# Performance work log

Hardware: AMD Instinct MI355X
Metric: run time of the kernel (lower is better)

## Reference

```python
import jax, jax.numpy as jnp
import numpy as np

N = 100000      # nodes (patches)
NNZ = 800000    # incidence (node, hyperedge) pairs from H.coo()
E = 16384       # hyperedges
IN = 128        # in_dim == hidden_dim (residual path active)
HID = 128
HEADS = 4
HD = HID // HEADS   # 32, per-head out_dim
QD = 64             # type_query_dim
L = 2               # n_layers
NT = 4              # n_node_types
ET = 3              # n_edge_types


def setup_inputs() -> dict:
    key = jax.random.key(0)
    ks = jax.random.split(key, 12)
    f32 = jnp.float32
    return {
        "x": jax.random.normal(ks[0], (N, IN), f32),
        "node_types": jax.random.randint(ks[1], (N,), 0, NT, jnp.int32),
        "node_idx": jax.random.randint(ks[2], (NNZ,), 0, N, jnp.int32),
        "edge_idx": jax.random.randint(ks[3], (NNZ,), 0, E, jnp.int32),
        "edge_type": jax.random.randint(ks[4], (E,), 0, ET, jnp.int32),
        # per-layer, per-head parameters (leading axes L, HEADS)
        "type_query": (jax.random.normal(ks[5], (L, HEADS, NT, QD), f32) * 0.02),
        "fc1_w": jax.random.normal(ks[6], (L, HEADS, IN + QD, 32), f32) / np.sqrt(IN + QD),
        "fc1_b": jnp.zeros((L, HEADS, 32), f32),
        "fc2_w": jax.random.normal(ks[7], (L, HEADS, 32, 1), f32) / np.sqrt(32.0),
        "fc2_b": jnp.zeros((L, HEADS, 1), f32),
        "Wq": jax.random.normal(ks[8], (L, HEADS, IN, HD), f32) / np.sqrt(IN),
        "Wv": jax.random.normal(ks[9], (L, HEADS, IN, HD), f32) / np.sqrt(IN),
        "edge_ctx": jax.random.normal(ks[10], (L, HEADS, ET, HD), f32) * 0.02,
        "ln_g": jnp.ones((L, HID), f32),
        "ln_b": jnp.zeros((L, HID), f32),
    }


def _seg_softmax(a, seg, num):
    # scatter_softmax over segments `seg` (stable: subtract per-segment max)
    m = jax.ops.segment_max(a, seg, num_segments=num)
    ex = jnp.exp(a - m[seg])
    s = jax.ops.segment_sum(ex, seg, num_segments=num)
    return ex / s[seg]


def _head(h, node_types, node_idx, edge_idx, edge_type, tq, w1, b1, w2, b2, wq, wv, ec):
    # CascadedHyperGAT.forward, one head
    sig = tq[node_types]                                      # (N, QD)
    z = jnp.tanh(jnp.concatenate([h, sig], axis=1) @ w1 + b1)  # (N, 32)
    alpha_type = jax.nn.sigmoid(z @ w2 + b2)[:, 0]             # (N,)
    Q = h @ wq                                                 # (N, HD)
    V = h @ wv                                                 # (N, HD)
    ctx = ec[edge_type][edge_idx]                              # (NNZ, HD)
    a = jnp.sum(Q[node_idx] * ctx, axis=1)                     # (NNZ,)
    a = jnp.where(a >= 0, a, 0.2 * a)                          # leaky_relu(0.2)
    a = a * alpha_type[node_idx]
    attn = _seg_softmax(a, edge_idx, E)                        # (NNZ,)
    edge_feat = jax.ops.segment_sum(attn[:, None] * V[node_idx], edge_idx, num_segments=E)
    node_feat = jax.ops.segment_sum(attn[:, None] * edge_feat[edge_idx], node_idx, num_segments=N)
    return node_feat, edge_feat


def _layernorm(h, g, b, eps=1e-5):
    mu = h.mean(-1, keepdims=True)
    var = ((h - mu) ** 2).mean(-1, keepdims=True)
    return (h - mu) * jax.lax.rsqrt(var + eps) * g + b


def reference(x, node_types, node_idx, edge_idx, edge_type,
              type_query, fc1_w, fc1_b, fc2_w, fc2_b, Wq, Wv, edge_ctx, ln_g, ln_b):
    head_v = jax.vmap(_head, in_axes=(None, None, None, None, None, 0, 0, 0, 0, 0, 0, 0, 0))
    stats = [x]
    h = x
    for l in range(L):  # small static layer count
        nf, _ = head_v(h, node_types, node_idx, edge_idx, edge_type,
                       type_query[l], fc1_w[l], fc1_b[l], fc2_w[l], fc2_b[l],
                       Wq[l], Wv[l], edge_ctx[l])            # (HEADS, N, HD)
        hn = jnp.transpose(nf, (1, 0, 2)).reshape(h.shape[0], -1)  # concat heads -> (N, HID)
        if hn.shape == h.shape:
            hn = hn + h                                       # residual (dims match)
        h = _layernorm(hn, ln_g[l], ln_b[l])
        stats.append(h)
    return jnp.concatenate(stats, axis=-1)                    # (N, IN + HID*L)
```

## Files before the change

### kernel.cpp

```cpp
#include <hip/hip_runtime.h>
#include <math.h>

#define HEADS 4
#define HD 32
#define QD 64
#define DIN 128
#define NTYPES 4
#define ETYPES 3
#define CAP 512
#define WTC 272

typedef __attribute__((ext_vector_type(8))) short bf16x8;
typedef __attribute__((ext_vector_type(4))) float f32x4;
typedef unsigned short ushort_t;

static inline int cdiv(int a, int b){ return (a + b - 1) / b; }

__device__ inline unsigned short f2bf(float f){
  unsigned u = __float_as_uint(f);
  unsigned r = (u + 0x7FFF + ((u >> 16) & 1)) >> 16;
  return (unsigned short)r;
}
__device__ inline float bf2f(unsigned short u){ return __uint_as_float(((unsigned)u) << 16); }

__device__ inline float lgt_get(const ushort_t* __restrict__ lgt, int n, int et, int hh){
  uint2 lg = *(const uint2*)((const char*)lgt + (size_t)n*24 + et*8);
  unsigned u = (hh & 2) ? lg.y : lg.x;
  return bf2f((hh & 1) ? (ushort_t)(u >> 16) : (ushort_t)(u & 0xffff));
}


__global__ __launch_bounds__(256) void hist_k(const int* __restrict__ node_idx,
                                              const int* __restrict__ edge_idx,
                                              int* __restrict__ cnt,
                                              uint2* __restrict__ ranks, int E, int NNZ)
{
  int i = blockIdx.x*256 + threadIdx.x;
  if (i < NNZ){
    unsigned re = (unsigned)atomicAdd(&cnt[edge_idx[i]], 1);
    unsigned rn = (unsigned)atomicAdd(&cnt[E + node_idx[i]], 1);
    uint2 r; r.x = re; r.y = rn;
    ranks[i] = r;
  }
}

__global__ __launch_bounds__(1024) void scan_pass1(const int* __restrict__ in, int* __restrict__ bsums, int n)
{
  __shared__ int sd[1024];
  int i = blockIdx.x*1024 + threadIdx.x;
  sd[threadIdx.x] = (i < n) ? in[i] : 0;
  __syncthreads();
  for (int s = 512; s > 0; s >>= 1){
    if (threadIdx.x < s) sd[threadIdx.x] += sd[threadIdx.x + s];
    __syncthreads();
  }
  if (threadIdx.x == 0) bsums[blockIdx.x] = sd[0];
}

__global__ __launch_bounds__(1024) void scan_pass2(int* __restrict__ bsums, int nb)
{
  __shared__ int sd[1024];
  int v = (threadIdx.x < nb) ? bsums[threadIdx.x] : 0;
  sd[threadIdx.x] = v;
  __syncthreads();
  for (int s = 1; s < 1024; s <<= 1){
    int t = (threadIdx.x >= s) ? sd[threadIdx.x - s] : 0;
    __syncthreads();
    sd[threadIdx.x] += t;
    __syncthreads();
  }
  if (threadIdx.x < nb) bsums[threadIdx.x] = sd[threadIdx.x] - v;
}

__global__ __launch_bounds__(1024) void scan_pass3(const int* __restrict__ in, const int* __restrict__ bsums,
                                                   int* __restrict__ out, int n)
{
  __shared__ int sd[1024];
  int i = blockIdx.x*1024 + threadIdx.x;
  int v = (i < n) ? in[i] : 0;
  sd[threadIdx.x] = v;
  __syncthreads();
  for (int s = 1; s < 1024; s <<= 1){
    int t = (threadIdx.x >= s) ? sd[threadIdx.x - s] : 0;
    __syncthreads();
    sd[threadIdx.x] += t;
    __syncthreads();
  }
  if (i < n) out[i] = bsums[blockIdx.x] + sd[threadIdx.x] - v;
}

__global__ __launch_bounds__(256) void scatter_k(const int* __restrict__ node_idx, const int* __restrict__ edge_idx,
                                                 const uint2* __restrict__ ranks,
                                                 const int* __restrict__ off,
                                                 uint2* __restrict__ srtE_rec, int E, int NNZ)
{
  int i = blockIdx.x*256 + threadIdx.x;
  if (i >= NNZ) return;
  int n = node_idx[i], e = edge_idx[i];
  uint2 r = ranks[i];
  int pe = off[e] + (int)r.x;
  int pn = off[E + n] - NNZ + (int)r.y;
  uint2 rec; rec.x = (unsigned)n; rec.y = (unsigned)pn;
  srtE_rec[pe] = rec;
}


__global__ __launch_bounds__(128) void wtprep_k(const float* __restrict__ w1, const float* __restrict__ wv,
                                                short* __restrict__ Wt, int L)
{
  int c = blockIdx.x % 256, l = blockIdx.x / 256;
  int k = threadIdx.x;
  int hh = (c >> 5) & 3, j = c & 31;
  float v;
  if (c < 128) v = w1[((((size_t)l*HEADS + hh)*(DIN+QD)) + k)*32 + j];
  else         v = wv[((((size_t)l*HEADS + hh)*DIN) + k)*32 + j];
  Wt[((size_t)l*WTC + c)*128 + k] = (short)f2bf(v);
}

__global__ __launch_bounds__(128) void wqc_k(const float* __restrict__ wq, const float* __restrict__ ec,
                                             short* __restrict__ Wt)
{
  int b = blockIdx.x;
  int l = b / 12, c = b % 12, h = c / 3, et = c % 3;
  int k = threadIdx.x;
  const float* wrow = wq + ((((size_t)l*HEADS + h)*DIN) + k)*32;
  const float* ecp  = ec + (((size_t)l*HEADS + h)*ETYPES + et)*32;
  float s = 0.f;
  #pragma unroll
  for (int d = 0; d < 32; d++) s += wrow[d] * ecp[d];
  Wt[((size_t)l*WTC + 256 + c)*128 + k] = (short)f2bf(s);
}

__global__ __launch_bounds__(32) void sbias_k(const float* __restrict__ tq, const float* __restrict__ w1,
                                              const float* __restrict__ b1, float* __restrict__ sbias)
{
  int b = blockIdx.x;
  int ty = b % NTYPES; int hh = (b / NTYPES) % HEADS; int l = b / (NTYPES*HEADS);
  int j = threadIdx.x;
  const float* tqp = tq + (((size_t)l*HEADS + hh)*NTYPES + ty)*QD;
  const float* w1p = w1 + ((size_t)l*HEADS + hh)*(DIN+QD)*32;
  float s = b1[((size_t)l*HEADS + hh)*32 + j];
  for (int k = 0; k < QD; k++) s += tqp[k] * w1p[(size_t)(DIN + k)*32 + j];
  sbias[(size_t)b*32 + j] = s;
}


__device__ inline void load_afrag(const float* __restrict__ h, int hstride, int N,
                                  int rbase, int mf, int l15, int l4, int kk, bf16x8& a)
{
  int row = rbase + mf*16 + l15;
  int rr = (row < N) ? row : (N-1);
  const float* pa = h + (size_t)rr*hstride + kk*32 + l4*8;
  float4 f0 = *(const float4*)pa;
  float4 f1 = *(const float4*)(pa + 4);
  a[0] = (short)f2bf(f0.x); a[1] = (short)f2bf(f0.y);
  a[2] = (short)f2bf(f0.z); a[3] = (short)f2bf(f0.w);
  a[4] = (short)f2bf(f1.x); a[5] = (short)f2bf(f1.y);
  a[6] = (short)f2bf(f1.z); a[7] = (short)f2bf(f1.w);
}


__global__ __launch_bounds__(256) void gemm_f2(
    const float* __restrict__ h, int hstride,
    const short* __restrict__ Wt,
    const int* __restrict__ node_types,
    const float* __restrict__ sbias,
    const float* __restrict__ w2,
    const float* __restrict__ b2,
    ushort_t* __restrict__ lgt,
    ushort_t* __restrict__ vb,
    int N)
{
  __shared__ float alds[64][HEADS];
  int lane = threadIdx.x & 63, wvid = threadIdx.x >> 6;
  int l15 = lane & 15, l4 = lane >> 4;
  int rbase = blockIdx.x*64;
  int wtcol0 = (wvid < 2) ? wvid*64 : (128 + (wvid - 2)*64);

  f32x4 acc[4][4] = {};
  f32x4 acc_e[4] = {};

  #pragma unroll
  for (int kk = 0; kk < 4; kk++){
    bf16x8 a[4], b[4];
    #pragma unroll
    for (int mf = 0; mf < 4; mf++) load_afrag(h, hstride, N, rbase, mf, l15, l4, kk, a[mf]);
    #pragma unroll
    for (int cf = 0; cf < 4; cf++){
      int col = wtcol0 + cf*16 + l15;
      b[cf] = *(const bf16x8*)(Wt + (size_t)col*128 + kk*32 + l4*8);
    }
    #pragma unroll
    for (int mf = 0; mf < 4; mf++)
      #pragma unroll
      for (int cf = 0; cf < 4; cf++)
        acc[mf][cf] = __builtin_amdgcn_mfma_f32_16x16x32_bf16(a[mf], b[cf], acc[mf][cf], 0, 0, 0);
    if (wvid == 0){
      int ecol = 256 + ((l15 < 12) ? l15 : 11);
      bf16x8 be = *(const bf16x8*)(Wt + (size_t)ecol*128 + kk*32 + l4*8);
      #pragma unroll
      for (int mf = 0; mf < 4; mf++)
        acc_e[mf] = __builtin_amdgcn_mfma_f32_16x16x32_bf16(a[mf], be, acc_e[mf], 0, 0, 0);
    }
  }

  if (wvid < 2){
    #pragma unroll
    for (int mf = 0; mf < 4; mf++){
      int rw[4], ty[4];
      #pragma unroll
      for (int r = 0; r < 4; r++){
        rw[r] = rbase + mf*16 + l4*4 + r;
        ty[r] = (rw[r] < N) ? node_types[rw[r]] : 0;
      }
      #pragma unroll
      for (int p = 0; p < 2; p++){
        int hh = wvid*2 + p;
        float w2a = w2[hh*32 + l15];
        float w2b = w2[hh*32 + 16 + l15];
        float b2v = b2[hh];
        #pragma unroll
        for (int r = 0; r < 4; r++){
          const float* sb = sbias + ((size_t)hh*NTYPES + ty[r])*32;
          float z0 = acc[mf][2*p  ][r] + sb[l15];
          float z1 = acc[mf][2*p+1][r] + sb[16 + l15];
          float t0 = 1.f - 2.f/(__expf(2.f*z0) + 1.f);
          float t1 = 1.f - 2.f/(__expf(2.f*z1) + 1.f);
          float val = t0*w2a + t1*w2b;
          val += __shfl_xor(val, 1); val += __shfl_xor(val, 2);
          val += __shfl_xor(val, 4); val += __shfl_xor(val, 8);
          if (l15 == 0)
            alds[mf*16 + l4*4 + r][hh] = 1.f/(1.f + __expf(-(val + b2v)));
        }
      }
    }
  } else {
    #pragma unroll
    for (int mf = 0; mf < 4; mf++){
      #pragma unroll
      for (int r = 0; r < 4; r++){
        int row = rbase + mf*16 + l4*4 + r;
        if (row < N){
          #pragma unroll
          for (int cf = 0; cf < 4; cf++){
            int c = (wvid - 2)*64 + cf*16 + l15;
            int hh = c >> 5, d = c & 31;
            vb[((size_t)hh*N + row)*32 + d] = f2bf(acc[mf][cf][r]);
          }
        }
      }
    }
  }
  __syncthreads();

  if (wvid == 0 && l15 < 12){
    int hq = l15 / 3, et = l15 % 3;
    #pragma unroll
    for (int mf = 0; mf < 4; mf++){
      #pragma unroll
      for (int r = 0; r < 4; r++){
        int rowloc = mf*16 + l4*4 + r;
        int row = rbase + rowloc;
        if (row < N){
          float s = acc_e[mf][r] * alds[rowloc][hq];
          s = (s >= 0.f) ? s : 0.2f*s;
          lgt[(size_t)row*12 + et*4 + hq] = f2bf(s);
        }
      }
    }
  }
}


__global__ __launch_bounds__(256) void k2b_f(
    const ushort_t* __restrict__ lgt, const ushort_t* __restrict__ vb,
    const uint2* __restrict__ srtE_rec, const int* __restrict__ edge_off, const int* __restrict__ cnt_e,
    const int* __restrict__ edge_type,
    ushort_t* __restrict__ efb,
    uint4* __restrict__ attn_rec,
    int N, int E)
{
  __shared__ float lbuf[HEADS][CAP];
  __shared__ int   nbuf[CAP];
  __shared__ int   pnbuf[CAP];
  __shared__ float mi[HEADS][2];

  int e = blockIdx.x;
  int off = edge_off[e], cnt = cnt_e[e];
  if (cnt == 0) return;
  int lane = threadIdx.x & 63, hh = threadIdx.x >> 6;
  int g = lane & 15, grp = lane >> 4;
  int et = edge_type[e];

  if (cnt <= CAP){
    for (int j = threadIdx.x; j < cnt; j += 256){
      uint2 rc = srtE_rec[off + j];
      uint2 lg = *(const uint2*)((const char*)lgt + (size_t)rc.x*24 + et*8);
      lbuf[0][j] = bf2f((ushort_t)(lg.x & 0xffff));
      lbuf[1][j] = bf2f((ushort_t)(lg.x >> 16));
      lbuf[2][j] = bf2f((ushort_t)(lg.y & 0xffff));
      lbuf[3][j] = bf2f((ushort_t)(lg.y >> 16));
      nbuf[j] = (int)rc.x;
      pnbuf[j] = (int)rc.y;
    }
    __syncthreads();

    float mloc = -INFINITY;
    for (int j = lane; j < cnt; j += 64) mloc = fmaxf(mloc, lbuf[hh][j]);
    #pragma unroll
    for (int sh = 32; sh > 0; sh >>= 1) mloc = fmaxf(mloc, __shfl_xor(mloc, sh));
    float m = mloc;

    float ef0 = 0.f, ef1 = 0.f, ssum = 0.f;
    const int cm1 = cnt - 1;
    const ushort_t* vbh = vb + (size_t)hh*N*32;
    for (int jj = 0; jj < cnt; jj += 16){
      int j0 = jj + grp, j1 = j0 + 4, j2 = j0 + 8, j3 = j0 + 12;
      int n0 = nbuf[(j0 < cm1) ? j0 : cm1];
      int n1 = nbuf[(j1 < cm1) ? j1 : cm1];
      int n2 = nbuf[(j2 < cm1) ? j2 : cm1];
      int n3 = nbuf[(j3 < cm1) ? j3 : cm1];
      unsigned w0 = *(const unsigned*)&vbh[(size_t)n0*32 + 2*g];
      unsigned w1 = *(const unsigned*)&vbh[(size_t)n1*32 + 2*g];
      unsigned w2 = *(const unsigned*)&vbh[(size_t)n2*32 + 2*g];
      unsigned w3 = *(const unsigned*)&vbh[(size_t)n3*32 + 2*g];
      float e0 = (j0 < cnt) ? __expf(lbuf[hh][j0] - m) : 0.f;
      float e1 = (j1 < cnt) ? __expf(lbuf[hh][j1] - m) : 0.f;
      float e2 = (j2 < cnt) ? __expf(lbuf[hh][j2] - m) : 0.f;
      float e3 = (j3 < cnt) ? __expf(lbuf[hh][j3] - m) : 0.f;
      ef0 += e0*bf2f((ushort_t)(w0 & 0xffff)) + e1*bf2f((ushort_t)(w1 & 0xffff))
           + e2*bf2f((ushort_t)(w2 & 0xffff)) + e3*bf2f((ushort_t)(w3 & 0xffff));
      ef1 += e0*bf2f((ushort_t)(w0 >> 16)) + e1*bf2f((ushort_t)(w1 >> 16))
           + e2*bf2f((ushort_t)(w2 >> 16)) + e3*bf2f((ushort_t)(w3 >> 16));
      ssum += e0 + e1 + e2 + e3;
    }
    ef0 += __shfl_xor(ef0, 16); ef0 += __shfl_xor(ef0, 32);
    ef1 += __shfl_xor(ef1, 16); ef1 += __shfl_xor(ef1, 32);
    ssum += __shfl_xor(ssum, 16); ssum += __shfl_xor(ssum, 32);
    float inv = 1.0f / ssum;
    if (grp == 0){
      unsigned w = (unsigned)f2bf(ef0*inv) | ((unsigned)f2bf(ef1*inv) << 16);
      *(unsigned*)&efb[(size_t)e*128 + hh*32 + 2*g] = w;
    }
    if (lane == 0){ mi[hh][0] = m; mi[hh][1] = inv; }
    __syncthreads();

    if (hh == 0){
      for (int j = lane; j < cnt; j += 64){
        int pn = pnbuf[j];
        float a0 = __expf(lbuf[0][j] - mi[0][0]) * mi[0][1];
        float a1 = __expf(lbuf[1][j] - mi[1][0]) * mi[1][1];
        float a2 = __expf(lbuf[2][j] - mi[2][0]) * mi[2][1];
        float a3 = __expf(lbuf[3][j] - mi[3][0]) * mi[3][1];
        uint4 o;
        o.x = (unsigned)e;
        o.y = (unsigned)f2bf(a0) | ((unsigned)f2bf(a1) << 16);
        o.z = (unsigned)f2bf(a2) | ((unsigned)f2bf(a3) << 16);
        o.w = 0u;
        attn_rec[pn] = o;
      }
    }
  } else {
    float mloc = -INFINITY;
    for (int j = lane; j < cnt; j += 64)
      mloc = fmaxf(mloc, lgt_get(lgt, (int)srtE_rec[off + j].x, et, hh));
    #pragma unroll
    for (int sh = 32; sh > 0; sh >>= 1) mloc = fmaxf(mloc, __shfl_xor(mloc, sh));
    float m = mloc;

    float ef0 = 0.f, ef1 = 0.f, ssum = 0.f;
    for (int jj = 0; jj < cnt; jj += 4){
      int j = jj + grp;
      if (j < cnt){
        int n = (int)srtE_rec[off + j].x;
        float ex = __expf(lgt_get(lgt, n, et, hh) - m);
        unsigned vw = *(const unsigned*)&vb[((size_t)hh*N + n)*32 + 2*g];
        ef0 += ex * bf2f((unsigned short)(vw & 0xffff));
        ef1 += ex * bf2f((unsigned short)(vw >> 16));
        ssum += ex;
      }
    }
    ef0 += __shfl_xor(ef0, 16); ef0 += __shfl_xor(ef0, 32);
    ef1 += __shfl_xor(ef1, 16); ef1 += __shfl_xor(ef1, 32);
    ssum += __shfl_xor(ssum, 16); ssum += __shfl_xor(ssum, 32);
    float inv = 1.0f / ssum;
    if (grp == 0){
      unsigned w = (unsigned)f2bf(ef0*inv) | ((unsigned)f2bf(ef1*inv) << 16);
      *(unsigned*)&efb[(size_t)e*128 + hh*32 + 2*g] = w;
    }
    for (int j = lane; j < cnt; j += 64){
      uint2 rc = srtE_rec[off + j];
      float ex = __expf(lgt_get(lgt, (int)rc.x, et, hh) - m);
      ushort_t* p = (ushort_t*)&attn_rec[rc.y];
      p[2 + hh] = f2bf(ex * inv);
      if (hh == 0){
        ((unsigned*)p)[0] = (unsigned)e;
        ((unsigned*)p)[3] = 0u;
      }
    }
  }
}


__global__ __launch_bounds__(256) void k2c(
    const uint4* __restrict__ attn_rec,
    const int* __restrict__ node_off, const int* __restrict__ cnt_n, int noff_shift,
    const ushort_t* __restrict__ efb,
    const float* __restrict__ h_in, int hstride,
    const float* __restrict__ ln_g, const float* __restrict__ ln_b,
    float* __restrict__ out, int out_stride, int out_col, int do_xcopy, int N, int E)
{
  int wv = threadIdx.x >> 6, lane = threadIdx.x & 63;
  int n = blockIdx.x*4 + wv;
  if (n >= N) return;
  int off = node_off[n] - noff_shift, cnt = cnt_n[n];
  int hh = lane >> 4;
  float nf0 = 0.f, nf1 = 0.f;

  for (int j0 = 0; j0 < cnt; j0 += 8){
    int mm = cnt - j0; if (mm > 8) mm = 8;
    uint4 rc = make_uint4(0u, 0u, 0u, 0u);
    if (lane < mm) rc = attn_rec[off + j0 + lane];
    unsigned w[8]; float av[8];
    #pragma unroll
    for (int j = 0; j < 8; j++){
      unsigned ej = (unsigned)__shfl((int)rc.x, j);
      unsigned ay = (unsigned)__shfl((int)rc.y, j);
      unsigned az = (unsigned)__shfl((int)rc.z, j);
      unsigned u = (hh & 2) ? az : ay;
      float a = bf2f((hh & 1) ? (ushort_t)(u >> 16) : (ushort_t)(u & 0xffff));
      av[j] = (j < mm) ? a : 0.f;
      w[j] = *(const unsigned*)&efb[(size_t)ej*128 + 2*lane];
    }
    #pragma unroll
    for (int j = 0; j < 8; j++){
      nf0 += av[j] * bf2f((ushort_t)(w[j] & 0xffff));
      nf1 += av[j] * bf2f((ushort_t)(w[j] >> 16));
    }
  }

  float2 hr = *(const float2*)&h_in[(size_t)n*hstride + 2*lane];
  if (do_xcopy)
    *(float2*)&out[(size_t)n*out_stride + 2*lane] = hr;
  float hn0 = nf0 + hr.x, hn1 = nf1 + hr.y;

  float s = hn0 + hn1;
  #pragma unroll
  for (int sh = 32; sh > 0; sh >>= 1) s += __shfl_xor(s, sh);
  float mu = s * (1.0f/128.0f);
  float d0 = hn0 - mu, d1 = hn1 - mu;
  float s2 = d0*d0 + d1*d1;
  #pragma unroll
  for (int sh = 32; sh > 0; sh >>= 1) s2 += __shfl_xor(s2, sh);
  float r = rsqrtf(s2*(1.0f/128.0f) + 1e-5f);

  float2 g2 = *(const float2*)&ln_g[2*lane];
  float2 b2 = *(const float2*)&ln_b[2*lane];
  float2 o2;
  o2.x = d0*r*g2.x + b2.x;
  o2.y = d1*r*g2.y + b2.y;
  *(float2*)&out[(size_t)n*out_stride + out_col + 2*lane] = o2;
}


extern "C" void kernel_launch(void* const* d_in, const int* in_sizes, int n_in,
                              void* d_out, int out_size, void* d_ws, size_t ws_size,
                              hipStream_t stream)
{
  const float* x          = (const float*)d_in[0];
  const int*   node_types = (const int*)  d_in[1];
  const int*   node_idx   = (const int*)  d_in[2];
  const int*   edge_idx   = (const int*)  d_in[3];
  const int*   edge_type  = (const int*)  d_in[4];
  const float* type_query = (const float*)d_in[5];
  const float* fc1_w      = (const float*)d_in[6];
  const float* fc1_b      = (const float*)d_in[7];
  const float* fc2_w      = (const float*)d_in[8];
  const float* fc2_b      = (const float*)d_in[9];
  const float* Wq         = (const float*)d_in[10];
  const float* Wv         = (const float*)d_in[11];
  const float* edge_ctx   = (const float*)d_in[12];
  const float* ln_g       = (const float*)d_in[13];
  const float* ln_b       = (const float*)d_in[14];

  const int N   = in_sizes[1];
  const int NNZ = in_sizes[2];
  const int E   = in_sizes[4];
  const int L   = 2;
  const int EN  = E + N;

  char* ws = (char*)d_ws;
  size_t o = 0;
  auto alloc = [&](size_t bytes)->void*{
    void* p = ws + o;
    o = (o + bytes + 255) & ~(size_t)255;
    return p;
  };
  int* cnt       = (int*)alloc((size_t)EN*4);
  int* off       = (int*)alloc((size_t)(EN+1)*4);
  uint2* ranks   = (uint2*)alloc((size_t)NNZ*8);
  uint2* srtE_rec= (uint2*)alloc((size_t)NNZ*8);
  int* bsum      = (int*)alloc((size_t)1024*4);
  uint4* attn_rec = (uint4*)alloc((size_t)NNZ*16);
  ushort_t* vb      = (ushort_t*)alloc((size_t)HEADS*N*32*2);
  ushort_t* lgt     = (ushort_t*)alloc((size_t)N*12*2);
  ushort_t* efb     = (ushort_t*)alloc((size_t)E*128*2);
  short*    Wt      = (short*)alloc((size_t)L*WTC*128*2);
  float*    sbias   = (float*)alloc((size_t)L*HEADS*NTYPES*32*4);
  if (o > ws_size) return;

  hipMemsetAsync(cnt, 0, (size_t)EN*4, stream);

  hist_k<<<cdiv(NNZ,256),256,0,stream>>>(node_idx, edge_idx, cnt, ranks, E, NNZ);

  int nb = cdiv(EN,1024);
  scan_pass1<<<nb,1024,0,stream>>>(cnt, bsum, EN);
  scan_pass2<<<1,1024,0,stream>>>(bsum, nb);
  scan_pass3<<<nb,1024,0,stream>>>(cnt, bsum, off, EN);

  scatter_k<<<cdiv(NNZ,256),256,0,stream>>>(node_idx, edge_idx, ranks, off, srtE_rec, E, NNZ);

  wtprep_k<<<L*256,128,0,stream>>>(fc1_w, Wv, Wt, L);
  wqc_k<<<L*12,128,0,stream>>>(Wq, edge_ctx, Wt);
  sbias_k<<<L*HEADS*NTYPES,32,0,stream>>>(type_query, fc1_w, fc1_b, sbias);

  for (int l = 0; l < L; l++){
    const float* hin = (l == 0) ? x : ((const float*)d_out + 128);
    int hstride = (l == 0) ? DIN : (3*DIN);

    gemm_f2<<<cdiv(N,64),256,0,stream>>>(
        hin, hstride,
        Wt + (size_t)l*WTC*128,
        node_types,
        sbias + (size_t)l*HEADS*NTYPES*32,
        fc2_w + (size_t)l*HEADS*32,
        fc2_b + (size_t)l*HEADS,
        lgt, vb, N);

    k2b_f<<<E,256,0,stream>>>(lgt, vb, srtE_rec, off, cnt,
                              edge_type, efb, attn_rec, N, E);

    k2c<<<cdiv(N,4),256,0,stream>>>(attn_rec, off + E, cnt + E, NNZ, efb,
                                    hin, hstride,
                                    ln_g + (size_t)l*DIN, ln_b + (size_t)l*DIN,
                                    (float*)d_out, 3*DIN, DIN + l*DIN, (l == 0) ? 1 : 0, N, E);
  }
}
```

Measured before the change: 554.8 us.

## Split fused projection GEMM into separate attention-logit and value kernels

After: 525.9 us, median of 2. -5.2%, faster.

```diff
diff --git a/kernel.cpp b/kernel.cpp
--- a/kernel.cpp
+++ b/kernel.cpp
@@ -160,7 +160,7 @@
 }
 
 
-__global__ __launch_bounds__(256) void gemm_f2(
+__global__ __launch_bounds__(256) void gemma_k(
     const float* __restrict__ h, int hstride,
     const short* __restrict__ Wt,
     const int* __restrict__ node_types,
@@ -168,14 +168,13 @@
     const float* __restrict__ w2,
     const float* __restrict__ b2,
     ushort_t* __restrict__ lgt,
-    ushort_t* __restrict__ vb,
     int N)
 {
-  __shared__ float alds[64][HEADS];
+  __shared__ float alds[128][HEADS];
   int lane = threadIdx.x & 63, wvid = threadIdx.x >> 6;
+  int wr = wvid >> 1, wc = wvid & 1;
   int l15 = lane & 15, l4 = lane >> 4;
-  int rbase = blockIdx.x*64;
-  int wtcol0 = (wvid < 2) ? wvid*64 : (128 + (wvid - 2)*64);
+  int rbase = blockIdx.x*128 + wr*64;
 
   f32x4 acc[4][4] = {};
   f32x4 acc_e[4] = {};
@@ -187,7 +186,7 @@
     for (int mf = 0; mf < 4; mf++) load_afrag(h, hstride, N, rbase, mf, l15, l4, kk, a[mf]);
     #pragma unroll
     for (int cf = 0; cf < 4; cf++){
-      int col = wtcol0 + cf*16 + l15;
+      int col = wc*64 + cf*16 + l15;
       b[cf] = *(const bf16x8*)(Wt + (size_t)col*128 + kk*32 + l4*8);
     }
     #pragma unroll
@@ -195,7 +194,7 @@
       #pragma unroll
       for (int cf = 0; cf < 4; cf++)
         acc[mf][cf] = __builtin_amdgcn_mfma_f32_16x16x32_bf16(a[mf], b[cf], acc[mf][cf], 0, 0, 0);
-    if (wvid == 0){
+    if (wc == 0){
       int ecol = 256 + ((l15 < 12) ? l15 : 11);
       bf16x8 be = *(const bf16x8*)(Wt + (size_t)ecol*128 + kk*32 + l4*8);
       #pragma unroll
@@ -204,67 +203,97 @@
     }
   }
 
-  if (wvid < 2){
-    #pragma unroll
-    for (int mf = 0; mf < 4; mf++){
-      int rw[4], ty[4];
+  #pragma unroll
+  for (int mf = 0; mf < 4; mf++){
+    int rw[4], ty[4];
+    #pragma unroll
+    for (int r = 0; r < 4; r++){
+      rw[r] = rbase + mf*16 + l4*4 + r;
+      ty[r] = (rw[r] < N) ? node_types[rw[r]] : 0;
+    }
+    #pragma unroll
+    for (int p = 0; p < 2; p++){
+      int hh = wc*2 + p;
+      float w2a = w2[hh*32 + l15];
+      float w2b = w2[hh*32 + 16 + l15];
+      float b2v = b2[hh];
       #pragma unroll
       for (int r = 0; r < 4; r++){
-        rw[r] = rbase + mf*16 + l4*4 + r;
-        ty[r] = (rw[r] < N) ? node_types[rw[r]] : 0;
+        const float* sb = sbias + ((size_t)hh*NTYPES + ty[r])*32;
+        float z0 = acc[mf][2*p  ][r] + sb[l15];
+        float z1 = acc[mf][2*p+1][r] + sb[16 + l15];
+        float t0 = 1.f - 2.f/(__expf(2.f*z0) + 1.f);
+        float t1 = 1.f - 2.f/(__expf(2.f*z1) + 1.f);
+        float val = t0*w2a + t1*w2b;
+        val += __shfl_xor(val, 1); val += __shfl_xor(val, 2);
+        val += __shfl_xor(val, 4); val += __shfl_xor(val, 8);
+        if (l15 == 0)
+          alds[wr*64 + mf*16 + l4*4 + r][hh] = 1.f/(1.f + __expf(-(val + b2v)));
       }
-      #pragma unroll
-      for (int p = 0; p < 2; p++){
-        int hh = wvid*2 + p;
-        float w2a = w2[hh*32 + l15];
-        float w2b = w2[hh*32 + 16 + l15];
-        float b2v = b2[hh];
-        #pragma unroll
-        for (int r = 0; r < 4; r++){
-          const float* sb = sbias + ((size_t)hh*NTYPES + ty[r])*32;
-          float z0 = acc[mf][2*p  ][r] + sb[l15];
-          float z1 = acc[mf][2*p+1][r] + sb[16 + l15];
-          float t0 = 1.f - 2.f/(__expf(2.f*z0) + 1.f);
-          float t1 = 1.f - 2.f/(__expf(2.f*z1) + 1.f);
-          float val = t0*w2a + t1*w2b;
-          val += __shfl_xor(val, 1); val += __shfl_xor(val, 2);
-          val += __shfl_xor(val, 4); val += __shfl_xor(val, 8);
-          if (l15 == 0)
-            alds[mf*16 + l4*4 + r][hh] = 1.f/(1.f + __expf(-(val + b2v)));
-        }
-      }
-    }
-  } else {
+    }
+  }
+  __syncthreads();
+
+  if (wc == 0 && l15 < 12){
+    int hq = l15 / 3, et = l15 % 3;
     #pragma unroll
     for (int mf = 0; mf < 4; mf++){
       #pragma unroll
       for (int r = 0; r < 4; r++){
-        int row = rbase + mf*16 + l4*4 + r;
-        if (row < N){
-          #pragma unroll
-          for (int cf = 0; cf < 4; cf++){
-            int c = (wvid - 2)*64 + cf*16 + l15;
-            int hh = c >> 5, d = c & 31;
-            vb[((size_t)hh*N + row)*32 + d] = f2bf(acc[mf][cf][r]);
-          }
-        }
-      }
-    }
-  }
-  __syncthreads();
-
-  if (wvid == 0 && l15 < 12){
-    int hq = l15 / 3, et = l15 % 3;
-    #pragma unroll
-    for (int mf = 0; mf < 4; mf++){
-      #pragma unroll
-      for (int r = 0; r < 4; r++){
-        int rowloc = mf*16 + l4*4 + r;
-        int row = rbase + rowloc;
+        int rowloc = wr*64 + mf*16 + l4*4 + r;
+        int row = blockIdx.x*128 + rowloc;
         if (row < N){
           float s = acc_e[mf][r] * alds[rowloc][hq];
           s = (s >= 0.f) ? s : 0.2f*s;
           lgt[(size_t)row*12 + et*4 + hq] = f2bf(s);
+        }
+      }
+    }
+  }
+}
+
+
+__global__ __launch_bounds__(256) void gemmv_k(
+    const float* __restrict__ h, int hstride,
+    const short* __restrict__ Wt,
+    ushort_t* __restrict__ vb,
+    int N)
+{
+  int lane = threadIdx.x & 63, wvid = threadIdx.x >> 6;
+  int wr = wvid >> 1, wc = wvid & 1;
+  int l15 = lane & 15, l4 = lane >> 4;
+  int rbase = blockIdx.x*128 + wr*64;
+
+  f32x4 acc[4][4] = {};
+
+  #pragma unroll
+  for (int kk = 0; kk < 4; kk++){
+    bf16x8 a[4], b[4];
+    #pragma unroll
+    for (int mf = 0; mf < 4; mf++) load_afrag(h, hstride, N, rbase, mf, l15, l4, kk, a[mf]);
+    #pragma unroll
+    for (int cf = 0; cf < 4; cf++){
+      int col = 128 + wc*64 + cf*16 + l15;
+      b[cf] = *(const bf16x8*)(Wt + (size_t)col*128 + kk*32 + l4*8);
+    }
+    #pragma unroll
+    for (int mf = 0; mf < 4; mf++)
+      #pragma unroll
+      for (int cf = 0; cf < 4; cf++)
+        acc[mf][cf] = __builtin_amdgcn_mfma_f32_16x16x32_bf16(a[mf], b[cf], acc[mf][cf], 0, 0, 0);
+  }
+
+  #pragma unroll
+  for (int mf = 0; mf < 4; mf++){
+    #pragma unroll
+    for (int r = 0; r < 4; r++){
+      int row = rbase + mf*16 + l4*4 + r;
+      if (row < N){
+        #pragma unroll
+        for (int cf = 0; cf < 4; cf++){
+          int c = wc*64 + cf*16 + l15;
+          int hh = c >> 5, d = c & 31;
+          vb[((size_t)hh*N + row)*32 + d] = f2bf(acc[mf][cf][r]);
         }
       }
     }
@@ -528,14 +557,19 @@
     const float* hin = (l == 0) ? x : ((const float*)d_out + 128);
     int hstride = (l == 0) ? DIN : (3*DIN);
 
-    gemm_f2<<<cdiv(N,64),256,0,stream>>>(
+    gemma_k<<<cdiv(N,128),256,0,stream>>>(
         hin, hstride,
         Wt + (size_t)l*WTC*128,
         node_types,
         sbias + (size_t)l*HEADS*NTYPES*32,
         fc2_w + (size_t)l*HEADS*32,
         fc2_b + (size_t)l*HEADS,
-        lgt, vb, N);
+        lgt, N);
+
+    gemmv_k<<<cdiv(N,128),256,0,stream>>>(
+        hin, hstride,
+        Wt + (size_t)l*WTC*128,
+        vb, N);
 
     k2b_f<<<E,256,0,stream>>>(lgt, vb, srtE_rec, off, cnt,
                               edge_type, efb, attn_rec, N, E);
```
